# Kernel tuning notes

Hardware: AMD Instinct MI355X
Metric: run time of the kernel (lower is better)

Reference implementation:

```python
import jax, jax.numpy as jnp
import numpy as np
import math

EMBED = 1024
HEADS = 16
HEAD_DIM = EMBED // HEADS
B, S = 4, 2048
FF = 4 * EMBED
EPS = 1e-5


def _layernorm(x, g, b):
    mu = jnp.mean(x, axis=-1, keepdims=True)
    var = jnp.mean(jnp.square(x - mu), axis=-1, keepdims=True)
    return (x - mu) * jax.lax.rsqrt(var + EPS) * g + b


def setup_inputs() -> dict:
    key = jax.random.key(0)
    ks = jax.random.split(key, 12)
    sd_e = 1.0 / math.sqrt(EMBED)
    sd_ff = 1.0 / math.sqrt(FF)
    return {
        "x": jax.random.normal(ks[0], (B, S, EMBED), jnp.float32),
        # attention weights stored [in, out] (transposed torch Linear)
        "Wq": jax.random.normal(ks[1], (EMBED, EMBED), jnp.float32) * sd_e,
        "bq": jnp.zeros((EMBED,), jnp.float32),
        "Wk": jax.random.normal(ks[2], (EMBED, EMBED), jnp.float32) * sd_e,
        "bk": jnp.zeros((EMBED,), jnp.float32),
        "Wv": jax.random.normal(ks[3], (EMBED, EMBED), jnp.float32) * sd_e,
        "bv": jnp.zeros((EMBED,), jnp.float32),
        "Wo": jax.random.normal(ks[4], (EMBED, EMBED), jnp.float32) * sd_e,
        "bo": jnp.zeros((EMBED,), jnp.float32),
        "g1": jnp.ones((EMBED,), jnp.float32),
        "beta1": jnp.zeros((EMBED,), jnp.float32),
        "g2": jnp.ones((EMBED,), jnp.float32),
        "beta2": jnp.zeros((EMBED,), jnp.float32),
        "W1": jax.random.normal(ks[5], (EMBED, FF), jnp.float32) * sd_e,
        "b1": jnp.zeros((FF,), jnp.float32),
        "W2": jax.random.normal(ks[6], (FF, EMBED), jnp.float32) * sd_ff,
        "b2": jnp.zeros((EMBED,), jnp.float32),
    }


def reference(x, Wq, bq, Wk, bk, Wv, bv, Wo, bo, g1, beta1, g2, beta2, W1, b1, W2, b2):
    b, s, _ = x.shape
    # --- pre-LN causal self-attention (dropout in eval = identity) ---
    h = _layernorm(x, g1, beta1)
    q = (h @ Wq + bq).reshape(b, s, HEADS, HEAD_DIM)
    k = (h @ Wk + bk).reshape(b, s, HEADS, HEAD_DIM)
    v = (h @ Wv + bv).reshape(b, s, HEADS, HEAD_DIM)
    scores = jnp.einsum("bqhd,bkhd->bhqk", q, k) / math.sqrt(HEAD_DIM)
    causal = jnp.tril(jnp.ones((s, s), bool))
    scores = jnp.where(causal, scores, jnp.float32(-1e8))
    attn = jax.nn.softmax(scores, axis=-1)
    y = jnp.einsum("bhqk,bkhd->bqhd", attn, v).reshape(b, s, EMBED)
    x = x + (y @ Wo + bo)
    # --- GELU MLP (exact erf gelu, torch default) ---
    h2 = _layernorm(x, g2, beta2)
    ff = jax.nn.gelu(h2 @ W1 + b1, approximate=False) @ W2 + b2
    return x + ff
```

## Files before the change

kernel.cpp:

```cpp
#include <hip/hip_runtime.h>
#include <hip/hip_bf16.h>
#include <stdint.h>
#include <math.h>

#define SEQ 2048
#define NTOK 8192
#define EMB 1024
#define NH 16
#define HD 64
#define FFD 4096
#define QSCALE 0.1803368801111137f

using us = unsigned short;
using b8 = __attribute__((ext_vector_type(8))) __bf16;
using f4 = __attribute__((ext_vector_type(4))) float;

__device__ __forceinline__ us f2b(float f) {
  union { float f; uint32_t u; } v; v.f = f;
  uint32_t u = v.u;
  return (us)((u + 0x7fffu + ((u >> 16) & 1u)) >> 16);
}

__device__ __forceinline__ uint32_t pkbf(float a, float b) {
  union { float f; uint32_t u; } x, y; x.f = a; y.f = b;
  return ((x.u + 0x8000u) >> 16) | ((y.u + 0x8000u) & 0xFFFF0000u);
}

__device__ __forceinline__ void async16(void* lds, const void* g) {
  __builtin_amdgcn_global_load_lds(
      (__attribute__((address_space(1))) void*)(uintptr_t)g,
      (__attribute__((address_space(3))) void*)(uintptr_t)lds, 16, 0, 0);
}

#define FENCED_BARRIER() do { asm volatile("" ::: "memory"); \
  __builtin_amdgcn_s_barrier(); asm volatile("" ::: "memory"); } while (0)

__device__ __forceinline__ float gelu_f(float x) {
  const float z = -2.30211416f * x * (1.f + 0.044715f * x * x);
  return x / (1.f + __builtin_amdgcn_exp2f(z));
}

__global__ __launch_bounds__(256)
void transpose_cast(const float* __restrict__ in, us* __restrict__ out, int R, int C,
                    float scale) {
  __shared__ float tile[32][33];
  const int bc = blockIdx.x * 32, br = blockIdx.y * 32;
  const int tx = threadIdx.x & 31, ty = threadIdx.x >> 5;
#pragma unroll
  for (int i = 0; i < 32; i += 8)
    tile[ty + i][tx] = in[(size_t)(br + ty + i) * C + bc + tx];
  __syncthreads();
#pragma unroll
  for (int i = 0; i < 32; i += 8)
    out[(size_t)(bc + ty + i) * R + br + tx] = f2b(tile[tx][ty + i] * scale);
}

__global__ void pack_bias(const float* __restrict__ bq, const float* __restrict__ bk,
                          const float* __restrict__ bv, float* __restrict__ o) {
  int i = blockIdx.x * 256 + threadIdx.x;
  o[i] = (i < 1024) ? bq[i] * QSCALE : (i < 2048 ? bk[i - 1024] : bv[i - 2048]);
}

__global__ __launch_bounds__(256)
void ln_kernel(const float* __restrict__ x, const float* __restrict__ g,
               const float* __restrict__ be, us* __restrict__ out) {
  __shared__ float red[8];
  const int row = blockIdx.x, t = threadIdx.x;
  const float4 v = ((const float4*)(x + (size_t)row * EMB))[t];
  float s = v.x + v.y + v.z + v.w;
  float s2 = v.x * v.x + v.y * v.y + v.z * v.z + v.w * v.w;
#pragma unroll
  for (int o = 32; o; o >>= 1) { s += __shfl_down(s, o, 64); s2 += __shfl_down(s2, o, 64); }
  if ((t & 63) == 0) { red[(t >> 6) * 2] = s; red[(t >> 6) * 2 + 1] = s2; }
  __syncthreads();
  const float ts = red[0] + red[2] + red[4] + red[6];
  const float ts2 = red[1] + red[3] + red[5] + red[7];
  const float mu = ts * (1.f / 1024.f);
  const float rs = rsqrtf(ts2 * (1.f / 1024.f) - mu * mu + 1e-5f);
  const float4 gv = ((const float4*)g)[t];
  const float4 bv = ((const float4*)be)[t];
  ushort4 o4;
  o4.x = f2b((v.x - mu) * rs * gv.x + bv.x);
  o4.y = f2b((v.y - mu) * rs * gv.y + bv.y);
  o4.z = f2b((v.z - mu) * rs * gv.z + bv.z);
  o4.w = f2b((v.w - mu) * rs * gv.w + bv.w);
  ((ushort4*)(out + (size_t)row * EMB))[t] = o4;
}

__global__ __launch_bounds__(512, 2)
void gemm256(const us* __restrict__ A, const us* __restrict__ Bt,
             const float* __restrict__ bias, us* __restrict__ outB,
             int N, int K, int gelu, int gy) {
  __shared__ us As[2][256 * 64];
  __shared__ us Bs[2][256 * 64];

  int bid = blockIdx.x;
  const int cpx = (int)gridDim.x >> 3;
  bid = (bid & 7) * cpx + (bid >> 3);
  const int bx = bid / gy, by = bid - bx * gy;
  const int row0 = bx * 256, col0 = by * 256;

  const int tid = threadIdx.x, w = tid >> 6, lane = tid & 63;
  const int wm = w >> 2, wn = w & 3;
  const int quad = lane >> 4, l15 = lane & 15;
  const int xr = l15 & 7;

  const int u0 = w * 2, u1 = u0 + 1;
  const int ar0 = ((u0 & 7) << 3) + ((u0 >> 3) << 7);
  const int ar1 = ((u1 & 7) << 3) + ((u1 >> 3) << 7);
  const int br0 = ((u0 & 3) << 3) + ((u0 >> 2) << 6);
  const int br1 = ((u1 & 3) << 3) + ((u1 >> 2) << 6);
  const int lrow = lane >> 3;
  const int loct = ((lane & 7) ^ lrow) << 3;
  const us* Ag0 = A + (size_t)(row0 + ar0 + lrow) * K + loct;
  const us* Ag1 = A + (size_t)(row0 + ar1 + lrow) * K + loct;
  const us* Bg0 = Bt + (size_t)(col0 + br0 + lrow) * K + loct;
  const us* Bg1 = Bt + (size_t)(col0 + br1 + lrow) * K + loct;
  const int NT = K >> 6;

  const f4 zf = {0.f, 0.f, 0.f, 0.f};
  f4 acc[8][4];
#pragma unroll
  for (int i = 0; i < 8; i++)
#pragma unroll
    for (int j = 0; j < 4; j++) acc[i][j] = zf;

  auto stgA = [&](int buf, int t, int mh) {
    const size_t go = (size_t)(mh << 6) * K + ((size_t)t << 6);
    async16(&As[buf][(ar0 + (mh << 6)) << 6], Ag0 + go);
    async16(&As[buf][(ar1 + (mh << 6)) << 6], Ag1 + go);
  };
  auto stgB = [&](int buf, int t, int nh) {
    const size_t go = (size_t)(nh << 5) * K + ((size_t)t << 6);
    async16(&Bs[buf][(br0 + (nh << 5)) << 6], Bg0 + go);
    async16(&Bs[buf][(br1 + (nh << 5)) << 6], Bg1 + go);
  };

  stgA(0, 0, 0); stgB(0, 0, 0); stgB(0, 0, 1); stgA(0, 0, 1);
  stgA(1, 1, 0); stgB(1, 1, 0); stgB(1, 1, 1);
  asm volatile("s_waitcnt vmcnt(6)" ::: "memory");
  FENCED_BARRIER();

  for (int t = 0; t < NT; t++) {
    const int cur = t & 1, nxt = cur ^ 1;
    const us* __restrict__ as = As[cur];
    const us* __restrict__ bs = Bs[cur];
    b8 af[2][4], bf0[2][2], bf1[2][2];

#pragma unroll
    for (int s = 0; s < 2; s++) {
      const int po = (((s << 2) + quad) ^ xr) << 3;
#pragma unroll
      for (int mi = 0; mi < 4; mi++)
        af[s][mi] = *(const b8*)&as[(wm * 128 + mi * 16 + l15) * 64 + po];
#pragma unroll
      for (int nf = 0; nf < 2; nf++)
        bf0[s][nf] = *(const b8*)&bs[(wn * 64 + nf * 16 + l15) * 64 + po];
    }
    if (t + 1 < NT) stgA(nxt, t + 1, 1);
    FENCED_BARRIER();
    asm volatile("s_waitcnt lgkmcnt(0)" ::: "memory");
    __builtin_amdgcn_s_setprio(1);
#pragma unroll
    for (int s = 0; s < 2; s++)
#pragma unroll
      for (int mi = 0; mi < 4; mi++)
#pragma unroll
        for (int nf = 0; nf < 2; nf++)
          acc[mi][nf] = __builtin_amdgcn_mfma_f32_16x16x32_bf16(af[s][mi], bf0[s][nf], acc[mi][nf], 0, 0, 0);
    __builtin_amdgcn_s_setprio(0);
    FENCED_BARRIER();

#pragma unroll
    for (int s = 0; s < 2; s++) {
      const int po = (((s << 2) + quad) ^ xr) << 3;
#pragma unroll
      for (int nf = 0; nf < 2; nf++)
        bf1[s][nf] = *(const b8*)&bs[(wn * 64 + 32 + nf * 16 + l15) * 64 + po];
    }
    if (t + 2 < NT) stgA(cur, t + 2, 0);
    FENCED_BARRIER();
    asm volatile("s_waitcnt lgkmcnt(0)" ::: "memory");
    __builtin_amdgcn_s_setprio(1);
#pragma unroll
    for (int s = 0; s < 2; s++)
#pragma unroll
      for (int mi = 0; mi < 4; mi++)
#pragma unroll
        for (int nf = 0; nf < 2; nf++)
          acc[mi][2 + nf] = __builtin_amdgcn_mfma_f32_16x16x32_bf16(af[s][mi], bf1[s][nf], acc[mi][2 + nf], 0, 0, 0);
    __builtin_amdgcn_s_setprio(0);
    FENCED_BARRIER();

#pragma unroll
    for (int s = 0; s < 2; s++) {
      const int po = (((s << 2) + quad) ^ xr) << 3;
#pragma unroll
      for (int mi = 0; mi < 4; mi++)
        af[s][mi] = *(const b8*)&as[(wm * 128 + 64 + mi * 16 + l15) * 64 + po];
    }
    if (t + 2 < NT) stgB(cur, t + 2, 0);
    FENCED_BARRIER();
    asm volatile("s_waitcnt lgkmcnt(0)" ::: "memory");
    __builtin_amdgcn_s_setprio(1);
#pragma unroll
    for (int s = 0; s < 2; s++)
#pragma unroll
      for (int mi = 0; mi < 4; mi++)
#pragma unroll
        for (int nf = 0; nf < 2; nf++)
          acc[4 + mi][nf] = __builtin_amdgcn_mfma_f32_16x16x32_bf16(af[s][mi], bf0[s][nf], acc[4 + mi][nf], 0, 0, 0);
    __builtin_amdgcn_s_setprio(0);
    FENCED_BARRIER();

    if (t + 2 < NT) {
      stgB(cur, t + 2, 1);
      asm volatile("s_waitcnt vmcnt(6)" ::: "memory");
    } else {
      asm volatile("s_waitcnt vmcnt(0)" ::: "memory");
    }
    FENCED_BARRIER();
    __builtin_amdgcn_s_setprio(1);
#pragma unroll
    for (int s = 0; s < 2; s++)
#pragma unroll
      for (int mi = 0; mi < 4; mi++)
#pragma unroll
        for (int nf = 0; nf < 2; nf++)
          acc[4 + mi][2 + nf] = __builtin_amdgcn_mfma_f32_16x16x32_bf16(af[s][mi], bf1[s][nf], acc[4 + mi][2 + nf], 0, 0, 0);
    __builtin_amdgcn_s_setprio(0);
    FENCED_BARRIER();
  }

#pragma unroll
  for (int mi8 = 0; mi8 < 8; mi8++)
#pragma unroll
    for (int nf = 0; nf < 4; nf++) {
      const int gcol = col0 + wn * 64 + nf * 16 + l15;
      const float bc = bias[gcol];
#pragma unroll
      for (int r = 0; r < 4; r++) {
        const int grow = row0 + wm * 128 + mi8 * 16 + quad * 4 + r;
        float v = acc[mi8][nf][r] + bc;
        if (gelu) v = gelu_f(v);
        outB[(size_t)grow * N + gcol] = f2b(v);
      }
    }
}

__global__ __launch_bounds__(512, 2)
void gemm128(const us* __restrict__ A, const us* __restrict__ Bt,
             const float* __restrict__ bias, const float* __restrict__ resid,
             float* __restrict__ outF, int N, int K, int gy) {
  __shared__ us As[2][128 * 64];
  __shared__ us Bs[2][256 * 64];

  int bid = blockIdx.x;
  const int cpx = (int)gridDim.x >> 3;
  bid = (bid & 7) * cpx + (bid >> 3);
  const int bx = bid / gy, by = bid - bx * gy;
  const int row0 = bx * 128, col0 = by * 256;

  const int tid = threadIdx.x, w = tid >> 6, lane = tid & 63;
  const int wm = w >> 2, wn = w & 3;
  const int quad = lane >> 4, l15 = lane & 15;
  const int xr = l15 & 7;

  const int u0 = w * 2, u1 = u0 + 1;
  const int aR0 = u0 << 3, aR1 = u1 << 3;
  const int bR0 = ((u0 & 3) << 3) + ((u0 >> 2) << 6);
  const int bR1 = ((u1 & 3) << 3) + ((u1 >> 2) << 6);
  const int lrow = lane >> 3;
  const int loct = ((lane & 7) ^ lrow) << 3;
  const us* Ag0 = A + (size_t)(row0 + aR0 + lrow) * K + loct;
  const us* Ag1 = A + (size_t)(row0 + aR1 + lrow) * K + loct;
  const us* Bg0 = Bt + (size_t)(col0 + bR0 + lrow) * K + loct;
  const us* Bg1 = Bt + (size_t)(col0 + bR1 + lrow) * K + loct;
  const int NT = K >> 6;

  const f4 zf = {0.f, 0.f, 0.f, 0.f};
  f4 acc[4][4];
#pragma unroll
  for (int i = 0; i < 4; i++)
#pragma unroll
    for (int j = 0; j < 4; j++) acc[i][j] = zf;

  auto stgA = [&](int buf, int t) {
    const size_t go = (size_t)t << 6;
    async16(&As[buf][aR0 << 6], Ag0 + go);
    async16(&As[buf][aR1 << 6], Ag1 + go);
  };
  auto stgB = [&](int buf, int t, int nh) {
    const size_t go = (size_t)(nh << 5) * K + ((size_t)t << 6);
    async16(&Bs[buf][(bR0 + (nh << 5)) << 6], Bg0 + go);
    async16(&Bs[buf][(bR1 + (nh << 5)) << 6], Bg1 + go);
  };

  stgA(0, 0); stgB(0, 0, 0); stgB(0, 0, 1);
  stgA(1, 1); stgB(1, 1, 0);
  asm volatile("s_waitcnt vmcnt(6)" ::: "memory");
  FENCED_BARRIER();

  for (int t = 0; t < NT; t++) {
    const int cur = t & 1, nxt = cur ^ 1;
    const us* __restrict__ as = As[cur];
    const us* __restrict__ bs = Bs[cur];
    b8 af[2][4], bf0[2][2], bf1[2][2];

#pragma unroll
    for (int s = 0; s < 2; s++) {
      const int po = (((s << 2) + quad) ^ xr) << 3;
#pragma unroll
      for (int mi = 0; mi < 4; mi++)
        af[s][mi] = *(const b8*)&as[(wm * 64 + mi * 16 + l15) * 64 + po];
#pragma unroll
      for (int nf = 0; nf < 2; nf++)
        bf0[s][nf] = *(const b8*)&bs[(wn * 64 + nf * 16 + l15) * 64 + po];
    }
    if (t + 1 < NT) {
      stgB(nxt, t + 1, 1);
      asm volatile("s_waitcnt vmcnt(6)" ::: "memory");
    } else {
      asm volatile("s_waitcnt vmcnt(0)" ::: "memory");
    }
    FENCED_BARRIER();
    asm volatile("s_waitcnt lgkmcnt(0)" ::: "memory");
    __builtin_amdgcn_s_setprio(1);
#pragma unroll
    for (int s = 0; s < 2; s++)
#pragma unroll
      for (int mi = 0; mi < 4; mi++)
#pragma unroll
        for (int nf = 0; nf < 2; nf++)
          acc[mi][nf] = __builtin_amdgcn_mfma_f32_16x16x32_bf16(af[s][mi], bf0[s][nf], acc[mi][nf], 0, 0, 0);
    __builtin_amdgcn_s_setprio(0);
    FENCED_BARRIER();

#pragma unroll
    for (int s = 0; s < 2; s++) {
      const int po = (((s << 2) + quad) ^ xr) << 3;
#pragma unroll
      for (int nf = 0; nf < 2; nf++)
        bf1[s][nf] = *(const b8*)&bs[(wn * 64 + 32 + nf * 16 + l15) * 64 + po];
    }
    if (t + 2 < NT) {
      stgA(cur, t + 2); stgB(cur, t + 2, 0);
      asm volatile("s_waitcnt vmcnt(6)" ::: "memory");
    } else {
      asm volatile("s_waitcnt vmcnt(2)" ::: "memory");
    }
    FENCED_BARRIER();
    asm volatile("s_waitcnt lgkmcnt(0)" ::: "memory");
    __builtin_amdgcn_s_setprio(1);
#pragma unroll
    for (int s = 0; s < 2; s++)
#pragma unroll
      for (int mi = 0; mi < 4; mi++)
#pragma unroll
        for (int nf = 0; nf < 2; nf++)
          acc[mi][2 + nf] = __builtin_amdgcn_mfma_f32_16x16x32_bf16(af[s][mi], bf1[s][nf], acc[mi][2 + nf], 0, 0, 0);
    __builtin_amdgcn_s_setprio(0);
    FENCED_BARRIER();
  }

#pragma unroll
  for (int mi = 0; mi < 4; mi++)
#pragma unroll
    for (int nf = 0; nf < 4; nf++) {
      const int gcol = col0 + wn * 64 + nf * 16 + l15;
      const float bc = bias[gcol];
#pragma unroll
      for (int r = 0; r < 4; r++) {
        const int grow = row0 + wm * 64 + mi * 16 + quad * 4 + r;
        outF[(size_t)grow * N + gcol] = acc[mi][nf][r] + bc + resid[(size_t)grow * N + gcol];
      }
    }
}

__global__ __launch_bounds__(256, 3)
void attn(const us* __restrict__ qkv, us* __restrict__ y) {
  static const signed char QTM[16] = {15,14,13,12, 10,11,8,9, 5,4,7,6, 0,1,2,3};
  const int bx = blockIdx.x;
  const int bh = bx & 63;
  const int qt = QTM[(bx >> 6) & 15];
  const int bb = bh >> 4, h = bh & 15;
  const int tid = threadIdx.x;
  const int wave = tid >> 6, lane = tid & 63;
  const int quad = lane >> 4, l15 = lane & 15;

  __shared__ us Ks[128 * 64];
  __shared__ us Vt[64 * 132];

  const size_t base = (size_t)bb * SEQ * 3072;
  const int q0 = qt * 128;

  b8 bqf[2][2];
#pragma unroll
  for (int qg = 0; qg < 2; qg++) {
    const us* qp = qkv + base + (size_t)(q0 + wave * 32 + qg * 16 + l15) * 3072 + h * 64 + quad * 8;
    bqf[qg][0] = *(const b8*)qp;
    bqf[qg][1] = *(const b8*)(qp + 32);
  }

  const f4 zf = {0.f, 0.f, 0.f, 0.f};
  f4 o[2][4];
  float mrow[2], lrow[2];
#pragma unroll
  for (int qg = 0; qg < 2; qg++) {
    mrow[qg] = -3.0e38f; lrow[qg] = 0.f;
#pragma unroll
    for (int dg = 0; dg < 4; dg++) o[qg][dg] = zf;
  }

  const int klr = lane >> 3, klc = lane & 7;
  const us* kgbase = qkv + base + (size_t)(wave * 32 + klr) * 3072 + 1024 + h * 64 + ((klc ^ klr) << 3);
  const us* vgbase = qkv + base + (size_t)(2 * lane) * 3072 + 2048 + h * 64 + wave * 8;

  float4 va0 = *(const float4*)(vgbase);
  float4 va1 = *(const float4*)(vgbase + 3072);
  float4 va2 = *(const float4*)(vgbase + 32);
  float4 va3 = *(const float4*)(vgbase + 3072 + 32);

  for (int kt = 0; kt <= qt; kt++) {
    const size_t koff = (size_t)kt * 128 * 3072;
#pragma unroll
    for (int op = 0; op < 4; op++)
      async16(&Ks[(wave * 32 + op * 8) * 64], kgbase + koff + (size_t)op * 8 * 3072);
    {
      union { float4 f; us u[8]; } v0, v1, v2, v3;
      v0.f = va0; v1.f = va1; v2.f = va2; v3.f = va3;
#pragma unroll
      for (int j = 0; j < 8; j++) {
        *(uint32_t*)&Vt[(wave * 8 + j) * 132 + 2 * lane] =
            (uint32_t)v0.u[j] | ((uint32_t)v1.u[j] << 16);
        *(uint32_t*)&Vt[(32 + wave * 8 + j) * 132 + 2 * lane] =
            (uint32_t)v2.u[j] | ((uint32_t)v3.u[j] << 16);
      }
    }
    float4 vb0, vb1, vb2, vb3;
    if (kt < qt) {
      const us* vg = vgbase + koff + (size_t)128 * 3072;
      vb0 = *(const float4*)(vg);
      vb1 = *(const float4*)(vg + 3072);
      vb2 = *(const float4*)(vg + 32);
      vb3 = *(const float4*)(vg + 3072 + 32);
      asm volatile("s_waitcnt vmcnt(4)" ::: "memory");
    } else {
      asm volatile("s_waitcnt vmcnt(0)" ::: "memory");
    }
    asm volatile("s_waitcnt lgkmcnt(0)" ::: "memory");
    FENCED_BARRIER();

    f4 sacc[2][8];
    __builtin_amdgcn_s_setprio(1);
#pragma unroll
    for (int c = 0; c < 8; c++) {
      const int krow = (c * 16 + l15) * 64;
      const int sw = l15 & 7;
      const b8 ak0 = *(const b8*)&Ks[krow + ((quad ^ sw) << 3)];
      const b8 ak1 = *(const b8*)&Ks[krow + (((quad ^ 4) ^ sw) << 3)];
#pragma unroll
      for (int qg = 0; qg < 2; qg++) {
        f4 s = __builtin_amdgcn_mfma_f32_16x16x32_bf16(ak0, bqf[qg][0], zf, 0, 0, 0);
        sacc[qg][c] = __builtin_amdgcn_mfma_f32_16x16x32_bf16(ak1, bqf[qg][1], s, 0, 0, 0);
      }
    }
    __builtin_amdgcn_s_setprio(0);

    uint32_t pf[2][16];
#pragma unroll
    for (int qg = 0; qg < 2; qg++) {
      const int q_in = wave * 32 + qg * 16 + l15;
      if (kt == qt) {
#pragma unroll
        for (int c = 0; c < 8; c++)
#pragma unroll
          for (int r = 0; r < 4; r++)
            if ((c * 16 + quad * 4 + r) > q_in) sacc[qg][c][r] = -3.0e38f;
      }
      float mx = sacc[qg][0][0];
#pragma unroll
      for (int c = 0; c < 8; c++)
#pragma unroll
        for (int r = 0; r < 4; r++) mx = fmaxf(mx, sacc[qg][c][r]);
      mx = fmaxf(mx, __shfl_xor(mx, 16, 64));
      mx = fmaxf(mx, __shfl_xor(mx, 32, 64));
      if (!__all(mx - mrow[qg] <= 8.f)) {
        const float mnew = fmaxf(mrow[qg], mx);
        const float al = __builtin_amdgcn_exp2f(mrow[qg] - mnew);
        mrow[qg] = mnew;
        lrow[qg] *= al;
#pragma unroll
        for (int r = 0; r < 4; r++) {
          const float ar = __shfl(al, quad * 4 + r, 64);
#pragma unroll
          for (int dg = 0; dg < 4; dg++) o[qg][dg][r] *= ar;
        }
      }
      const float mb = mrow[qg];
      float rs = 0.f;
#pragma unroll
      for (int c = 0; c < 8; c++) {
        const float p0 = __builtin_amdgcn_exp2f(sacc[qg][c][0] - mb);
        const float p1 = __builtin_amdgcn_exp2f(sacc[qg][c][1] - mb);
        const float p2 = __builtin_amdgcn_exp2f(sacc[qg][c][2] - mb);
        const float p3 = __builtin_amdgcn_exp2f(sacc[qg][c][3] - mb);
        rs += (p0 + p1) + (p2 + p3);
        pf[qg][c * 2] = pkbf(p0, p1);
        pf[qg][c * 2 + 1] = pkbf(p2, p3);
      }
      rs += __shfl_xor(rs, 16, 64);
      rs += __shfl_xor(rs, 32, 64);
      lrow[qg] += rs;
    }

    __builtin_amdgcn_s_setprio(1);
#pragma unroll
    for (int c = 0; c < 8; c++) {
      union { uint32_t w[4]; b8 v; } af0, af1;
      af0.w[0] = pf[0][c * 2]; af0.w[1] = pf[0][c * 2 + 1]; af0.w[2] = 0u; af0.w[3] = 0u;
      af1.w[0] = pf[1][c * 2]; af1.w[1] = pf[1][c * 2 + 1]; af1.w[2] = 0u; af1.w[3] = 0u;
#pragma unroll
      for (int dg = 0; dg < 4; dg++) {
        const uint2 vd = *(const uint2*)&Vt[(dg * 16 + l15) * 132 + c * 16 + quad * 4];
        union { uint32_t w[4]; b8 v; } vb;
        vb.w[0] = vd.x; vb.w[1] = vd.y; vb.w[2] = 0u; vb.w[3] = 0u;
        o[0][dg] = __builtin_amdgcn_mfma_f32_16x16x32_bf16(af0.v, vb.v, o[0][dg], 0, 0, 0);
        o[1][dg] = __builtin_amdgcn_mfma_f32_16x16x32_bf16(af1.v, vb.v, o[1][dg], 0, 0, 0);
      }
    }
    __builtin_amdgcn_s_setprio(0);
    asm volatile("s_waitcnt lgkmcnt(0)" ::: "memory");
    FENCED_BARRIER();
    if (kt < qt) {
      va0 = vb0; va1 = vb1; va2 = vb2; va3 = vb3;
    }
  }

#pragma unroll
  for (int qg = 0; qg < 2; qg++) {
    float lr[4];
#pragma unroll
    for (int r = 0; r < 4; r++) lr[r] = __shfl(lrow[qg], quad * 4 + r, 64);
#pragma unroll
    for (int dg = 0; dg < 4; dg++)
#pragma unroll
      for (int r = 0; r < 4; r++) {
        const int gq = q0 + wave * 32 + qg * 16 + quad * 4 + r;
        y[(size_t)(bb * SEQ + gq) * EMB + h * 64 + dg * 16 + l15] = f2b(o[qg][dg][r] / lr[r]);
      }
  }
}

extern "C" void kernel_launch(void* const* d_in, const int* in_sizes, int n_in,
                              void* d_out, int out_size, void* d_ws, size_t ws_size,
                              hipStream_t stream) {
  const float* x = (const float*)d_in[0];
  const float* Wq = (const float*)d_in[1];
  const float* bq = (const float*)d_in[2];
  const float* Wk = (const float*)d_in[3];
  const float* bk = (const float*)d_in[4];
  const float* Wv = (const float*)d_in[5];
  const float* bv = (const float*)d_in[6];
  const float* Wo = (const float*)d_in[7];
  const float* bo = (const float*)d_in[8];
  const float* g1 = (const float*)d_in[9];
  const float* be1 = (const float*)d_in[10];
  const float* g2 = (const float*)d_in[11];
  const float* be2 = (const float*)d_in[12];
  const float* W1 = (const float*)d_in[13];
  const float* b1 = (const float*)d_in[14];
  const float* W2 = (const float*)d_in[15];
  const float* b2 = (const float*)d_in[16];
  float* out = (float*)d_out;

  char* ws = (char*)d_ws;
  const size_t MB = 1024ull * 1024ull;
  us* WqkvT = (us*)(ws + 0);
  us* WoT   = (us*)(ws + 6 * MB);
  us* W1T   = (us*)(ws + 8 * MB);
  us* W2T   = (us*)(ws + 16 * MB);
  us* hbuf  = (us*)(ws + 24 * MB);
  us* qkvb  = (us*)(ws + 40 * MB);
  us* ybuf  = (us*)(ws + 88 * MB);
  float* x1 = (float*)(ws + 104 * MB);
  us* h2    = (us*)(ws + 136 * MB);
  us* ff1   = (us*)(ws + 24 * MB);
  float* bqkv = (float*)(ws + 152 * MB);

  transpose_cast<<<dim3(32, 32), 256, 0, stream>>>(Wq, WqkvT, 1024, 1024, QSCALE);
  transpose_cast<<<dim3(32, 32), 256, 0, stream>>>(Wk, WqkvT + 1024 * 1024, 1024, 1024, 1.f);
  transpose_cast<<<dim3(32, 32), 256, 0, stream>>>(Wv, WqkvT + 2 * 1024 * 1024, 1024, 1024, 1.f);
  transpose_cast<<<dim3(32, 32), 256, 0, stream>>>(Wo, WoT, 1024, 1024, 1.f);
  transpose_cast<<<dim3(128, 32), 256, 0, stream>>>(W1, W1T, 1024, 4096, 1.f);
  transpose_cast<<<dim3(32, 128), 256, 0, stream>>>(W2, W2T, 4096, 1024, 1.f);
  pack_bias<<<12, 256, 0, stream>>>(bq, bk, bv, bqkv);

  ln_kernel<<<NTOK, 256, 0, stream>>>(x, g1, be1, hbuf);
  gemm256<<<dim3(384), 512, 0, stream>>>(hbuf, WqkvT, bqkv, qkvb, 3072, 1024, 0, 12);
  attn<<<1024, 256, 0, stream>>>(qkvb, ybuf);
  gemm128<<<dim3(256), 512, 0, stream>>>(ybuf, WoT, bo, x, x1, 1024, 1024, 4);
  ln_kernel<<<NTOK, 256, 0, stream>>>(x1, g2, be2, h2);
  gemm256<<<dim3(512), 512, 0, stream>>>(h2, W1T, b1, ff1, 4096, 1024, 1, 16);
  gemm128<<<dim3(256), 512, 0, stream>>>(ff1, W2T, b2, x1, out, 1024, 4096, 4);
}
```

Baseline: 519.7 us.

## Fuse weight prep and first layernorm into one launch; double-buffer V tile in attention

Merges the six transpose-cast launches, the bias pack and the first layernorm into one kernel that dispatches on block index. This removes per-launch overhead and lets the small weight transposes overlap with the layernorm. Separately, the attention kernel gets a double-buffered V tile in LDS. The next V tile is written to the spare buffer after softmax, moving the transposed store off the critical path at the start of each iteration, at the cost of extra LDS per block and a vmcnt(0) wait mid-iteration.

```diff
diff --git a/kernel.cpp b/kernel.cpp
--- a/kernel.cpp
+++ b/kernel.cpp
@@ -41,24 +41,71 @@
 }
 
 __global__ __launch_bounds__(256)
-void transpose_cast(const float* __restrict__ in, us* __restrict__ out, int R, int C,
-                    float scale) {
+void prep(const float* __restrict__ Wq, const float* __restrict__ Wk,
+          const float* __restrict__ Wv, const float* __restrict__ Wo,
+          const float* __restrict__ W1, const float* __restrict__ W2,
+          const float* __restrict__ bq, const float* __restrict__ bk,
+          const float* __restrict__ bv,
+          const float* __restrict__ x, const float* __restrict__ g1,
+          const float* __restrict__ be1,
+          us* __restrict__ WqkvT, us* __restrict__ WoT, us* __restrict__ W1T,
+          us* __restrict__ W2T, float* __restrict__ bqkv, us* __restrict__ hbuf) {
   __shared__ float tile[32][33];
-  const int bc = blockIdx.x * 32, br = blockIdx.y * 32;
-  const int tx = threadIdx.x & 31, ty = threadIdx.x >> 5;
-#pragma unroll
-  for (int i = 0; i < 32; i += 8)
-    tile[ty + i][tx] = in[(size_t)(br + ty + i) * C + bc + tx];
-  __syncthreads();
-#pragma unroll
-  for (int i = 0; i < 32; i += 8)
-    out[(size_t)(bc + ty + i) * R + br + tx] = f2b(tile[tx][ty + i] * scale);
-}
-
-__global__ void pack_bias(const float* __restrict__ bq, const float* __restrict__ bk,
-                          const float* __restrict__ bv, float* __restrict__ o) {
-  int i = blockIdx.x * 256 + threadIdx.x;
-  o[i] = (i < 1024) ? bq[i] * QSCALE : (i < 2048 ? bk[i - 1024] : bv[i - 2048]);
+  __shared__ float red[8];
+  const int bid = blockIdx.x;
+  const int t = threadIdx.x;
+
+  if (bid < 12288) {
+    int R, C, csh, t0; const float* in; us* out; float sc = 1.f;
+    if (bid < 4096) {
+      R = 1024; C = 1024; csh = 5; t0 = bid & 1023;
+      const int m = bid >> 10;
+      in  = (m == 0) ? Wq : (m == 1) ? Wk : (m == 2) ? Wv : Wo;
+      out = (m == 0) ? WqkvT : (m == 1) ? (WqkvT + (1 << 20))
+          : (m == 2) ? (WqkvT + (2 << 20)) : WoT;
+      if (m == 0) sc = QSCALE;
+    } else if (bid < 8192) {
+      R = 1024; C = 4096; csh = 7; t0 = bid - 4096; in = W1; out = W1T;
+    } else {
+      R = 4096; C = 1024; csh = 5; t0 = bid - 8192; in = W2; out = W2T;
+    }
+    const int bc = (t0 & ((1 << csh) - 1)) << 5;
+    const int br = (t0 >> csh) << 5;
+    const int tx = t & 31, ty = t >> 5;
+#pragma unroll
+    for (int i = 0; i < 32; i += 8)
+      tile[ty + i][tx] = in[(size_t)(br + ty + i) * C + bc + tx];
+    __syncthreads();
+#pragma unroll
+    for (int i = 0; i < 32; i += 8)
+      out[(size_t)(bc + ty + i) * R + br + tx] = f2b(tile[tx][ty + i] * sc);
+
+  } else if (bid < 12300) {
+    const int i = (bid - 12288) * 256 + t;
+    bqkv[i] = (i < 1024) ? bq[i] * QSCALE : (i < 2048 ? bk[i - 1024] : bv[i - 2048]);
+
+  } else {
+    const int row = bid - 12300;
+    const float4 v = ((const float4*)(x + (size_t)row * EMB))[t];
+    float s = v.x + v.y + v.z + v.w;
+    float s2 = v.x * v.x + v.y * v.y + v.z * v.z + v.w * v.w;
+#pragma unroll
+    for (int o = 32; o; o >>= 1) { s += __shfl_down(s, o, 64); s2 += __shfl_down(s2, o, 64); }
+    if ((t & 63) == 0) { red[(t >> 6) * 2] = s; red[(t >> 6) * 2 + 1] = s2; }
+    __syncthreads();
+    const float ts = red[0] + red[2] + red[4] + red[6];
+    const float ts2 = red[1] + red[3] + red[5] + red[7];
+    const float mu = ts * (1.f / 1024.f);
+    const float rs = rsqrtf(ts2 * (1.f / 1024.f) - mu * mu + 1e-5f);
+    const float4 gv = ((const float4*)g1)[t];
+    const float4 bv4 = ((const float4*)be1)[t];
+    ushort4 o4;
+    o4.x = f2b((v.x - mu) * rs * gv.x + bv4.x);
+    o4.y = f2b((v.y - mu) * rs * gv.y + bv4.y);
+    o4.z = f2b((v.z - mu) * rs * gv.z + bv4.z);
+    o4.w = f2b((v.w - mu) * rs * gv.w + bv4.w);
+    ((ushort4*)(hbuf + (size_t)row * EMB))[t] = o4;
+  }
 }
 
 __global__ __launch_bounds__(256)
@@ -389,7 +436,7 @@
   const int quad = lane >> 4, l15 = lane & 15;
 
   __shared__ us Ks[128 * 64];
-  __shared__ us Vt[64 * 132];
+  __shared__ us Vt[2][64 * 132];
 
   const size_t base = (size_t)bb * SEQ * 3072;
   const int q0 = qt * 128;
@@ -416,27 +463,27 @@
   const us* kgbase = qkv + base + (size_t)(wave * 32 + klr) * 3072 + 1024 + h * 64 + ((klc ^ klr) << 3);
   const us* vgbase = qkv + base + (size_t)(2 * lane) * 3072 + 2048 + h * 64 + wave * 8;
 
-  float4 va0 = *(const float4*)(vgbase);
-  float4 va1 = *(const float4*)(vgbase + 3072);
-  float4 va2 = *(const float4*)(vgbase + 32);
-  float4 va3 = *(const float4*)(vgbase + 3072 + 32);
+  {
+    union { float4 f; us u[8]; } v0, v1, v2, v3;
+    v0.f = *(const float4*)(vgbase);
+    v1.f = *(const float4*)(vgbase + 3072);
+    v2.f = *(const float4*)(vgbase + 32);
+    v3.f = *(const float4*)(vgbase + 3072 + 32);
+#pragma unroll
+    for (int j = 0; j < 8; j++) {
+      *(uint32_t*)&Vt[0][(wave * 8 + j) * 132 + 2 * lane] =
+          (uint32_t)v0.u[j] | ((uint32_t)v1.u[j] << 16);
+      *(uint32_t*)&Vt[0][(32 + wave * 8 + j) * 132 + 2 * lane] =
+          (uint32_t)v2.u[j] | ((uint32_t)v3.u[j] << 16);
+    }
+  }
 
   for (int kt = 0; kt <= qt; kt++) {
+    const int cur = kt & 1, nxt = cur ^ 1;
     const size_t koff = (size_t)kt * 128 * 3072;
 #pragma unroll
     for (int op = 0; op < 4; op++)
       async16(&Ks[(wave * 32 + op * 8) * 64], kgbase + koff + (size_t)op * 8 * 3072);
-    {
-      union { float4 f; us u[8]; } v0, v1, v2, v3;
-      v0.f = va0; v1.f = va1; v2.f = va2; v3.f = va3;
-#pragma unroll
-      for (int j = 0; j < 8; j++) {
-        *(uint32_t*)&Vt[(wave * 8 + j) * 132 + 2 * lane] =
-            (uint32_t)v0.u[j] | ((uint32_t)v1.u[j] << 16);
-        *(uint32_t*)&Vt[(32 + wave * 8 + j) * 132 + 2 * lane] =
-            (uint32_t)v2.u[j] | ((uint32_t)v3.u[j] << 16);
-      }
-    }
     float4 vb0, vb1, vb2, vb3;
     if (kt < qt) {
       const us* vg = vgbase + koff + (size_t)128 * 3072;
@@ -514,6 +561,19 @@
       lrow[qg] += rs;
     }
 
+    if (kt < qt) {
+      asm volatile("s_waitcnt vmcnt(0)" ::: "memory");
+      union { float4 f; us u[8]; } v0, v1, v2, v3;
+      v0.f = vb0; v1.f = vb1; v2.f = vb2; v3.f = vb3;
+#pragma unroll
+      for (int j = 0; j < 8; j++) {
+        *(uint32_t*)&Vt[nxt][(wave * 8 + j) * 132 + 2 * lane] =
+            (uint32_t)v0.u[j] | ((uint32_t)v1.u[j] << 16);
+        *(uint32_t*)&Vt[nxt][(32 + wave * 8 + j) * 132 + 2 * lane] =
+            (uint32_t)v2.u[j] | ((uint32_t)v3.u[j] << 16);
+      }
+    }
+
     __builtin_amdgcn_s_setprio(1);
 #pragma unroll
     for (int c = 0; c < 8; c++) {
@@ -522,7 +582,7 @@
       af1.w[0] = pf[1][c * 2]; af1.w[1] = pf[1][c * 2 + 1]; af1.w[2] = 0u; af1.w[3] = 0u;
 #pragma unroll
       for (int dg = 0; dg < 4; dg++) {
-        const uint2 vd = *(const uint2*)&Vt[(dg * 16 + l15) * 132 + c * 16 + quad * 4];
+        const uint2 vd = *(const uint2*)&Vt[cur][(dg * 16 + l15) * 132 + c * 16 + quad * 4];
         union { uint32_t w[4]; b8 v; } vb;
         vb.w[0] = vd.x; vb.w[1] = vd.y; vb.w[2] = 0u; vb.w[3] = 0u;
         o[0][dg] = __builtin_amdgcn_mfma_f32_16x16x32_bf16(af0.v, vb.v, o[0][dg], 0, 0, 0);
@@ -532,9 +592,6 @@
     __builtin_amdgcn_s_setprio(0);
     asm volatile("s_waitcnt lgkmcnt(0)" ::: "memory");
     FENCED_BARRIER();
-    if (kt < qt) {
-      va0 = vb0; va1 = vb1; va2 = vb2; va3 = vb3;
-    }
   }
 
 #pragma unroll
@@ -588,15 +645,9 @@
   us* ff1   = (us*)(ws + 24 * MB);
   float* bqkv = (float*)(ws + 152 * MB);
 
-  transpose_cast<<<dim3(32, 32), 256, 0, stream>>>(Wq, WqkvT, 1024, 1024, QSCALE);
-  transpose_cast<<<dim3(32, 32), 256, 0, stream>>>(Wk, WqkvT + 1024 * 1024, 1024, 1024, 1.f);
-  transpose_cast<<<dim3(32, 32), 256, 0, stream>>>(Wv, WqkvT + 2 * 1024 * 1024, 1024, 1024, 1.f);
-  transpose_cast<<<dim3(32, 32), 256, 0, stream>>>(Wo, WoT, 1024, 1024, 1.f);
-  transpose_cast<<<dim3(128, 32), 256, 0, stream>>>(W1, W1T, 1024, 4096, 1.f);
-  transpose_cast<<<dim3(32, 128), 256, 0, stream>>>(W2, W2T, 4096, 1024, 1.f);
-  pack_bias<<<12, 256, 0, stream>>>(bq, bk, bv, bqkv);
-
-  ln_kernel<<<NTOK, 256, 0, stream>>>(x, g1, be1, hbuf);
+  prep<<<dim3(20492), 256, 0, stream>>>(Wq, Wk, Wv, Wo, W1, W2, bq, bk, bv,
+                                        x, g1, be1,
+                                        WqkvT, WoT, W1T, W2T, bqkv, hbuf);
   gemm256<<<dim3(384), 512, 0, stream>>>(hbuf, WqkvT, bqkv, qkvb, 3072, 1024, 0, 12);
   attn<<<1024, 256, 0, stream>>>(qkvb, ybuf);
   gemm128<<<dim3(256), 512, 0, stream>>>(ybuf, WoT, bo, x, x1, 1024, 1024, 4);
```

Result: faster. 486.7 us (-6.3%).
